# Kernel optimization log

Hardware: AMD Instinct MI355X
Metric: run time of the kernel (lower is better)

The kernel has to match this reference:

```python
import jax, jax.numpy as jnp
import numpy as np

N_NODES = 50000
N_GRAPHS = 64


def gcn_layer(x, W, b, src, dst, norm, n):
    # PyG GCNConv: h = x @ W; aggregate norm-weighted messages at dst; add bias
    h = x @ W
    msg = h[src] * norm[:, None]          # [E_tot, out_dim] gather
    out = jax.ops.segment_sum(msg, dst, num_segments=n)
    return out + b


def to_dense_batch(x, batch, max_num, num_graphs):
    n = x.shape[0]
    counts = jax.ops.segment_sum(jnp.ones((n,), x.dtype), batch, num_segments=num_graphs)
    starts = jnp.concatenate([jnp.zeros((1,), jnp.int32),
                              jnp.cumsum(counts.astype(jnp.int32))[:-1]])
    pos = jnp.arange(n, dtype=jnp.int32) - starts[batch]
    valid = pos < max_num
    b_idx = jnp.where(valid, batch, num_graphs)   # overflow -> dummy row
    p_idx = jnp.where(valid, pos, 0)
    dense = jnp.zeros((num_graphs + 1, max_num, x.shape[1]), x.dtype)
    dense = dense.at[b_idx, p_idx].set(x)
    return dense[:num_graphs]


def setup_inputs() -> dict:
    key = jax.random.key(0)
    ks = jax.random.split(key, 12)
    F0, F2, F3, OUT = 54, 108, 216, 200
    x = jax.random.normal(ks[0], (N_NODES, F0), jnp.float32)
    edge_index = jax.random.randint(ks[1], (2, 800000), 0, N_NODES, jnp.int64)
    batch = jnp.sort(jax.random.randint(ks[2], (N_NODES,), 0, N_GRAPHS, jnp.int64))
    def glorot(k, shp):
        lim = 1.0 / np.sqrt(shp[0])
        return jax.random.uniform(k, shp, jnp.float32, -lim, lim)
    return {
        "x": x, "edge_index": edge_index, "batch": batch, "max_num": 1000,
        "W1": glorot(ks[3], (F0, F0)), "b1": jnp.zeros((F0,), jnp.float32),
        "W2": glorot(ks[4], (F0, F2)), "b2": jnp.zeros((F2,), jnp.float32),
        "W3": glorot(ks[5], (F2, F3)), "b3": jnp.zeros((F3,), jnp.float32),
        "Wf": glorot(ks[6], (F3, OUT)), "bf": glorot(ks[7], (OUT,)),
    }


def reference(x, edge_index, batch, max_num, W1, b1, W2, b2, W3, b3, Wf, bf):
    n = x.shape[0]
    loops = jnp.arange(n, dtype=edge_index.dtype)
    src = jnp.concatenate([edge_index[0], loops])
    dst = jnp.concatenate([edge_index[1], loops])
    # symmetric GCN normalization with self-loops (edge_weight = 1)
    deg = jax.ops.segment_sum(jnp.ones_like(dst, jnp.float32), dst, num_segments=n)
    dinv = jax.lax.rsqrt(deg)  # deg >= 1 due to self-loops
    norm = dinv[src] * dinv[dst]

    h = jax.nn.relu(gcn_layer(x, W1, b1, src, dst, norm, n))
    h = jax.nn.relu(gcn_layer(h, W2, b2, src, dst, norm, n))
    h = jax.nn.relu(gcn_layer(h, W3, b3, src, dst, norm, n))
    h = h @ Wf + bf
    return to_dense_batch(h, batch, max_num, N_GRAPHS)
```

## Files before the change

kernel.cpp:

```cpp
#include <hip/hip_runtime.h>
#include <hip/hip_bf16.h>

#define N_GRAPHS 64

typedef __bf16 bf16x8 __attribute__((ext_vector_type(8)));
typedef float floatx4 __attribute__((ext_vector_type(4)));
typedef unsigned short ushort8v __attribute__((ext_vector_type(8)));

__device__ __forceinline__ float b2f(unsigned short u) {
    union { unsigned int i; float f; } v;
    v.i = ((unsigned int)u) << 16;
    return v.f;
}
__device__ __forceinline__ unsigned short f2b(float f) {
    __hip_bfloat16 h = __float2bfloat16(f);
    return *(unsigned short*)&h;
}


__global__ void k_deg(const int* __restrict__ dst, int* __restrict__ deg, int E) {
    int e = blockIdx.x * blockDim.x + threadIdx.x;
    if (e < E) atomicAdd(&deg[dst[e]], 1);
}

__global__ void k_scan_blocks(const int* __restrict__ deg, int* __restrict__ row_start,
                              int* __restrict__ blk_sums, int N) {
    __shared__ int s[256];
    int t = threadIdx.x;
    int i = blockIdx.x * 256 + t;
    int v = (i < N) ? deg[i] : 0;
    s[t] = v;
    __syncthreads();
    for (int off = 1; off < 256; off <<= 1) {
        int x = (t >= off) ? s[t - off] : 0;
        __syncthreads();
        s[t] += x;
        __syncthreads();
    }
    if (i < N) row_start[i] = s[t] - v;
    if (t == 255) blk_sums[blockIdx.x] = s[255];
}

__global__ void k_scan_tot(const int* __restrict__ blk_sums, int nb, int* __restrict__ blk_off) {
    __shared__ int s[256];
    int t = threadIdx.x;
    int v = (t < nb) ? blk_sums[t] : 0;
    s[t] = v;
    __syncthreads();
    for (int off = 1; off < 256; off <<= 1) {
        int x = (t >= off) ? s[t - off] : 0;
        __syncthreads();
        s[t] += x;
        __syncthreads();
    }
    if (t < nb) blk_off[t] = s[t] - v;
}

__global__ void k_scan_add(int* __restrict__ row_start, const int* __restrict__ blk_off,
                           int* __restrict__ cursor, const int* __restrict__ deg,
                           float* __restrict__ dinv, const int* __restrict__ batch,
                           int* __restrict__ gstarts, int N, int E) {
    int i = blockIdx.x * 256 + threadIdx.x;
    if (i < N) {
        int r = row_start[i] + blk_off[blockIdx.x];
        row_start[i] = r;
        cursor[i] = r;
        dinv[i] = 1.0f / sqrtf((float)(deg[i] + 1));
        int b = batch[i];
        int prev = (i == 0) ? -1 : batch[i - 1];
        for (int g = prev + 1; g <= b; ++g) gstarts[g] = i;
        if (i == N - 1)
            for (int g = b + 1; g <= N_GRAPHS; ++g) gstarts[g] = N;
    }
    if (i == 0) row_start[N] = E;
}

__global__ void k_fill(const int* __restrict__ src, const int* __restrict__ dst,
                       int* __restrict__ cursor, int2* __restrict__ col2,
                       const float* __restrict__ dinv, int E) {
    int e = blockIdx.x * blockDim.x + threadIdx.x;
    if (e < E) {
        int s = src[e];
        int p = atomicAdd(&cursor[dst[e]], 1);
        col2[p] = make_int2(s, __float_as_int(dinv[s]));
    }
}

__device__ __forceinline__ void swz_one(const float* __restrict__ W,
                                        unsigned short* __restrict__ Wsw, int i, int K, int Nn,
                                        int KS) {
    int j = i & 7, lane = (i >> 3) & 63;
    int ks = (i >> 9) % KS, nt = i / (512 * KS);
    int n = nt * 16 + (lane & 15);
    int k = ks * 32 + (lane >> 4) * 8 + j;
    float v = (k < K && n < Nn) ? W[(size_t)k * Nn + n] : 0.f;
    Wsw[i] = f2b(v);
}

#define T_W1 (4 * 2 * 512)
#define T_W2 (8 * 2 * 512)
#define T_W3 (14 * 4 * 512)
#define T_WF (13 * 7 * 512)

__global__ void k_prep(const float* __restrict__ W1, const float* __restrict__ W2,
                       const float* __restrict__ W3, const float* __restrict__ Wf,
                       unsigned short* __restrict__ W1s, unsigned short* __restrict__ W2s,
                       unsigned short* __restrict__ W3s, unsigned short* __restrict__ Wfs,
                       const float* __restrict__ x, unsigned short* __restrict__ xb, int Nn) {
    int i = blockIdx.x * 256 + threadIdx.x;
    if (i < T_W1) swz_one(W1, W1s, i, 54, 54, 2);
    else if (i < T_W1 + T_W2) swz_one(W2, W2s, i - T_W1, 54, 108, 2);
    else if (i < T_W1 + T_W2 + T_W3) swz_one(W3, W3s, i - T_W1 - T_W2, 108, 216, 4);
    else if (i < T_W1 + T_W2 + T_W3 + T_WF)
        swz_one(Wf, Wfs, i - T_W1 - T_W2 - T_W3, 216, 200, 7);
    else {
        int ii = i - (T_W1 + T_W2 + T_W3 + T_WF);
        if (ii < Nn * 64) {
            int n = ii >> 6, c = ii & 63;
            xb[ii] = (c < 54) ? f2b(x[(size_t)n * 54 + c]) : (unsigned short)0;
        }
    }
}


template <int P, int AS, int NODES, int NG>
__device__ __forceinline__ void gatherP(const unsigned short* __restrict__ in,
                                        const int* __restrict__ row_start,
                                        const int2* __restrict__ col2,
                                        const float* __restrict__ dinv,
                                        unsigned short* agg_s, int node0, int N, int t) {
    constexpr int S = P / 8;
    constexpr int G = 32 / S;
    constexpr int RPG = NODES / NG;
    int grp = t >> 5, lane5 = t & 31;
    int j = lane5 / S, cl = lane5 % S;
    int rs_a[RPG], re_a[RPG];
    float dn_a[RPG];
#pragma unroll
    for (int rr = 0; rr < RPG; ++rr) {
        int n = node0 + grp + rr * NG;
        bool valid = n < N;
        rs_a[rr] = valid ? row_start[n] : 0;
        re_a[rr] = valid ? row_start[n + 1] : 0;
        dn_a[rr] = valid ? dinv[n] : 0.f;
    }
#pragma unroll
    for (int rr = 0; rr < RPG; ++rr) {
        int r = grp + rr * NG;
        int n = node0 + r;
        float a[8] = {0.f, 0.f, 0.f, 0.f, 0.f, 0.f, 0.f, 0.f};
        if (n < N) {
            float dn = dn_a[rr];
            if (j == 0) {
                ushort8v u = *((const ushort8v*)(in + (size_t)n * P) + cl);
#pragma unroll
                for (int i = 0; i < 8; ++i) a[i] = dn * b2f(u[i]);
            }
            int re = re_a[rr];
            int e = rs_a[rr] + j;
            for (; e < re; e += 4 * G) {
                int e1 = min(e + G, re - 1);
                int e2 = min(e + 2 * G, re - 1);
                int e3 = min(e + 3 * G, re - 1);
                int2 c0 = col2[e];
                int2 c1 = col2[e1];
                int2 c2 = col2[e2];
                int2 c3 = col2[e3];
                ushort8v v0 = *((const ushort8v*)(in + (size_t)c0.x * P) + cl);
                ushort8v v1 = *((const ushort8v*)(in + (size_t)c1.x * P) + cl);
                ushort8v v2 = *((const ushort8v*)(in + (size_t)c2.x * P) + cl);
                ushort8v v3 = *((const ushort8v*)(in + (size_t)c3.x * P) + cl);
                float d0 = __int_as_float(c0.y);
                float d1 = (e + G < re) ? __int_as_float(c1.y) : 0.f;
                float d2 = (e + 2 * G < re) ? __int_as_float(c2.y) : 0.f;
                float d3 = (e + 3 * G < re) ? __int_as_float(c3.y) : 0.f;
#pragma unroll
                for (int i = 0; i < 8; ++i) {
                    a[i] += d0 * b2f(v0[i]) + d1 * b2f(v1[i]);
                    a[i] += d2 * b2f(v2[i]) + d3 * b2f(v3[i]);
                }
            }
#pragma unroll
            for (int i = 0; i < 8; ++i) a[i] *= dn;
        }
#pragma unroll
        for (int mask = S; mask < 32; mask <<= 1)
#pragma unroll
            for (int i = 0; i < 8; ++i) a[i] += __shfl_xor(a[i], mask, 32);
        if (j == 0) {
            ushort8v rv;
#pragma unroll
            for (int i = 0; i < 8; ++i) rv[i] = f2b(a[i]);
            *((ushort8v*)(agg_s + r * AS) + cl) = rv;
        }
    }
}


template <int P, int FOUT, int FP, int KS, int NT>
__global__ __launch_bounds__(256) void k_layer(
    const unsigned short* __restrict__ in, const int* __restrict__ row_start,
    const int2* __restrict__ col2, const float* __restrict__ dinv,
    const unsigned short* __restrict__ Wsw, const float* __restrict__ bias,
    unsigned short* __restrict__ hout, int N) {
    constexpr int AS = KS * 32 + 8;
    __shared__ __align__(16) unsigned short agg_s[16 * AS];
    int node0 = blockIdx.x * 16;
    int t = threadIdx.x;
    gatherP<P, AS, 16, 8>(in, row_start, col2, dinv, agg_s, node0, N, t);
    __syncthreads();
    int lane = t & 63, wv = t >> 6, m = lane & 15, q = lane >> 4;
    bf16x8 a[KS];
#pragma unroll
    for (int ks = 0; ks < KS; ++ks)
        a[ks] = *(const bf16x8*)(agg_s + m * AS + ks * 32 + q * 8);
    for (int nt = wv; nt < NT; nt += 4) {
        const unsigned short* bp = Wsw + ((size_t)(nt * KS) * 64 + lane) * 8;
        bf16x8 bfr[KS];
#pragma unroll
        for (int ks = 0; ks < KS; ++ks) bfr[ks] = *(const bf16x8*)(bp + ks * 512);
        int fo = nt * 16 + m;
        float bb = (fo < FOUT) ? bias[fo] : 0.f;
        floatx4 c = {0.f, 0.f, 0.f, 0.f};
#pragma unroll
        for (int ks = 0; ks < KS; ++ks)
            c = __builtin_amdgcn_mfma_f32_16x16x32_bf16(a[ks], bfr[ks], c, 0, 0, 0);
#pragma unroll
        for (int r = 0; r < 4; ++r) {
            int n = node0 + q * 4 + r;
            if (n < N) hout[(size_t)n * FP + fo] = f2b(fmaxf(c[r] + bb, 0.f));
        }
    }
}


__global__ __launch_bounds__(256) void k_l3f(
    const unsigned short* __restrict__ h2, const int* __restrict__ row_start,
    const int2* __restrict__ col2, const float* __restrict__ dinv,
    const unsigned short* __restrict__ W3s, const float* __restrict__ b3,
    const unsigned short* __restrict__ Wfs, const float* __restrict__ bfv,
    const int* __restrict__ batch, const int* __restrict__ gstarts, float* __restrict__ out,
    int N, int mn) {
    constexpr int AS = 136, HS = 232;
    __shared__ __align__(16) unsigned short smem[32 * HS];
    unsigned short* agg_s = smem;
    unsigned short* h3_s = smem;
    int node0 = blockIdx.x * 32;
    int t = threadIdx.x;
    gatherP<128, AS, 32, 8>(h2, row_start, col2, dinv, agg_s, node0, N, t);
    __syncthreads();
    int lane = t & 63, wv = t >> 6, m = lane & 15, q = lane >> 4;
    bf16x8 a1[2][4];
#pragma unroll
    for (int mt = 0; mt < 2; ++mt)
#pragma unroll
        for (int ks = 0; ks < 4; ++ks)
            a1[mt][ks] = *(const bf16x8*)(agg_s + (mt * 16 + m) * AS + ks * 32 + q * 8);
    __syncthreads();
    for (int nt = wv; nt < 14; nt += 4) {
        const unsigned short* bp = W3s + ((size_t)(nt * 4) * 64 + lane) * 8;
        bf16x8 bf0 = *(const bf16x8*)(bp);
        bf16x8 bf1 = *(const bf16x8*)(bp + 512);
        bf16x8 bf2 = *(const bf16x8*)(bp + 1024);
        bf16x8 bf3 = *(const bf16x8*)(bp + 1536);
        int fo = nt * 16 + m;
        float bb = (fo < 216) ? b3[fo] : 0.f;
#pragma unroll
        for (int mt = 0; mt < 2; ++mt) {
            floatx4 c = {0.f, 0.f, 0.f, 0.f};
            c = __builtin_amdgcn_mfma_f32_16x16x32_bf16(a1[mt][0], bf0, c, 0, 0, 0);
            c = __builtin_amdgcn_mfma_f32_16x16x32_bf16(a1[mt][1], bf1, c, 0, 0, 0);
            c = __builtin_amdgcn_mfma_f32_16x16x32_bf16(a1[mt][2], bf2, c, 0, 0, 0);
            c = __builtin_amdgcn_mfma_f32_16x16x32_bf16(a1[mt][3], bf3, c, 0, 0, 0);
#pragma unroll
            for (int r = 0; r < 4; ++r) {
                int row = mt * 16 + q * 4 + r;
                h3_s[row * HS + fo] = f2b(fmaxf(c[r] + bb, 0.f));
            }
        }
    }
    __syncthreads();
    bf16x8 a2[2][7];
#pragma unroll
    for (int mt = 0; mt < 2; ++mt)
#pragma unroll
        for (int ks = 0; ks < 7; ++ks)
            a2[mt][ks] = *(const bf16x8*)(h3_s + (mt * 16 + m) * HS + ks * 32 + q * 8);
    for (int nt = wv; nt < 13; nt += 4) {
        const unsigned short* bp = Wfs + ((size_t)(nt * 7) * 64 + lane) * 8;
        bf16x8 bfr[7];
#pragma unroll
        for (int ks = 0; ks < 7; ++ks) bfr[ks] = *(const bf16x8*)(bp + ks * 512);
        int fo = nt * 16 + m;
        if (fo >= 200) continue;
        float bb = bfv[fo];
#pragma unroll
        for (int mt = 0; mt < 2; ++mt) {
            floatx4 c = {0.f, 0.f, 0.f, 0.f};
#pragma unroll
            for (int ks = 0; ks < 7; ++ks)
                c = __builtin_amdgcn_mfma_f32_16x16x32_bf16(a2[mt][ks], bfr[ks], c, 0, 0, 0);
#pragma unroll
            for (int r = 0; r < 4; ++r) {
                int n = node0 + mt * 16 + q * 4 + r;
                if (n < N) {
                    int b = batch[n];
                    int pos = n - gstarts[b];
                    if (pos >= 0 && pos < mn)
                        out[((size_t)b * mn + pos) * 200 + fo] = c[r] + bb;
                }
            }
        }
    }
}

extern "C" void kernel_launch(void* const* d_in, const int* in_sizes, int n_in,
                              void* d_out, int out_size, void* d_ws, size_t ws_size,
                              hipStream_t stream) {
    const float* x = (const float*)d_in[0];
    const int* ei = (const int*)d_in[1];
    const int* batch = (const int*)d_in[2];
    const float* W1 = (const float*)d_in[4];
    const float* b1 = (const float*)d_in[5];
    const float* W2 = (const float*)d_in[6];
    const float* b2 = (const float*)d_in[7];
    const float* W3 = (const float*)d_in[8];
    const float* b3 = (const float*)d_in[9];
    const float* Wf = (const float*)d_in[10];
    const float* bfv = (const float*)d_in[11];
    float* out = (float*)d_out;

    const int N = in_sizes[2];
    const int E = in_sizes[1] / 2;
    const int mn = out_size / (N_GRAPHS * 200);
    const int* src = ei;
    const int* dst = ei + E;

    char* w = (char*)d_ws;
    auto alloc = [&](size_t bytes) {
        void* p = (void*)w;
        w += (bytes + 255) & ~(size_t)255;
        return p;
    };
    int* deg = (int*)alloc((size_t)N * 4);
    int* row_start = (int*)alloc((size_t)(N + 1) * 4);
    int* blk_sums = (int*)alloc(256 * 4);
    int* blk_off = (int*)alloc(256 * 4);
    int* cursor = (int*)alloc((size_t)N * 4);
    int2* col2 = (int2*)alloc((size_t)E * 8);
    float* dinv = (float*)alloc((size_t)N * 4);
    int* gstarts = (int*)alloc((N_GRAPHS + 1) * 4);
    unsigned short* xb = (unsigned short*)alloc((size_t)N * 64 * 2);
    unsigned short* h1 = (unsigned short*)alloc((size_t)N * 64 * 2);
    unsigned short* h2 = (unsigned short*)alloc((size_t)N * 128 * 2);
    unsigned short* W1s = (unsigned short*)alloc((size_t)T_W1 * 2);
    unsigned short* W2s = (unsigned short*)alloc((size_t)T_W2 * 2);
    unsigned short* W3s = (unsigned short*)alloc((size_t)T_W3 * 2);
    unsigned short* Wfs = (unsigned short*)alloc((size_t)T_WF * 2);
    (void)ws_size;

    hipMemsetAsync(deg, 0, (size_t)N * 4, stream);
    hipMemsetAsync(d_out, 0, (size_t)out_size * sizeof(float), stream);

    int NB = (N + 255) / 256;
    k_deg<<<(E + 255) / 256, 256, 0, stream>>>(dst, deg, E);
    k_scan_blocks<<<NB, 256, 0, stream>>>(deg, row_start, blk_sums, N);
    k_scan_tot<<<1, 256, 0, stream>>>(blk_sums, NB, blk_off);
    k_scan_add<<<NB, 256, 0, stream>>>(row_start, blk_off, cursor, deg, dinv, batch, gstarts,
                                       N, E);
    k_fill<<<(E + 255) / 256, 256, 0, stream>>>(src, dst, cursor, col2, dinv, E);
    int prep_total = T_W1 + T_W2 + T_W3 + T_WF + N * 64;
    k_prep<<<(prep_total + 255) / 256, 256, 0, stream>>>(W1, W2, W3, Wf, W1s, W2s, W3s, Wfs,
                                                         x, xb, N);

    int NBL16 = (N + 15) / 16;
    k_layer<64, 54, 64, 2, 4><<<NBL16, 256, 0, stream>>>(xb, row_start, col2, dinv, W1s, b1,
                                                         h1, N);
    k_layer<64, 108, 128, 2, 8><<<NBL16, 256, 0, stream>>>(h1, row_start, col2, dinv, W2s,
                                                           b2, h2, N);
    int NBL32 = (N + 31) / 32;
    k_l3f<<<NBL32, 256, 0, stream>>>(h2, row_start, col2, dinv, W3s, b3, Wfs, bfv, batch,
                                     gstarts, out, N, mn);
}
```

Baseline: 304.5 us.

## Merge degree count with weight prep and fill with padding-only output zeroing

Fuses the edge degree-count kernel with the weight swizzle/x conversion kernel into one launch, and fuses the CSR fill kernel with a new zeroing pass that clears only the padded tail rows of each graph in the dense output. This replaces a full-output memset with zeroing of just the rows the final layer does not write, and drops two launches. It relies on the final kernel writing every valid row, since those rows are no longer pre-zeroed.

```diff
diff --git a/kernel.cpp b/kernel.cpp
--- a/kernel.cpp
+++ b/kernel.cpp
@@ -17,11 +17,6 @@
     return *(unsigned short*)&h;
 }
 
-
-__global__ void k_deg(const int* __restrict__ dst, int* __restrict__ deg, int E) {
-    int e = blockIdx.x * blockDim.x + threadIdx.x;
-    if (e < E) atomicAdd(&deg[dst[e]], 1);
-}
 
 __global__ void k_scan_blocks(const int* __restrict__ deg, int* __restrict__ row_start,
                               int* __restrict__ blk_sums, int N) {
@@ -75,17 +70,6 @@
     if (i == 0) row_start[N] = E;
 }
 
-__global__ void k_fill(const int* __restrict__ src, const int* __restrict__ dst,
-                       int* __restrict__ cursor, int2* __restrict__ col2,
-                       const float* __restrict__ dinv, int E) {
-    int e = blockIdx.x * blockDim.x + threadIdx.x;
-    if (e < E) {
-        int s = src[e];
-        int p = atomicAdd(&cursor[dst[e]], 1);
-        col2[p] = make_int2(s, __float_as_int(dinv[s]));
-    }
-}
-
 __device__ __forceinline__ void swz_one(const float* __restrict__ W,
                                         unsigned short* __restrict__ Wsw, int i, int K, int Nn,
                                         int KS) {
@@ -102,12 +86,19 @@
 #define T_W3 (14 * 4 * 512)
 #define T_WF (13 * 7 * 512)
 
-__global__ void k_prep(const float* __restrict__ W1, const float* __restrict__ W2,
-                       const float* __restrict__ W3, const float* __restrict__ Wf,
-                       unsigned short* __restrict__ W1s, unsigned short* __restrict__ W2s,
-                       unsigned short* __restrict__ W3s, unsigned short* __restrict__ Wfs,
-                       const float* __restrict__ x, unsigned short* __restrict__ xb, int Nn) {
-    int i = blockIdx.x * 256 + threadIdx.x;
+__global__ void k_deg_prep(const int* __restrict__ dst, int* __restrict__ deg, int E, int EB,
+                           const float* __restrict__ W1, const float* __restrict__ W2,
+                           const float* __restrict__ W3, const float* __restrict__ Wf,
+                           unsigned short* __restrict__ W1s, unsigned short* __restrict__ W2s,
+                           unsigned short* __restrict__ W3s, unsigned short* __restrict__ Wfs,
+                           const float* __restrict__ x, unsigned short* __restrict__ xb,
+                           int Nn) {
+    if ((int)blockIdx.x < EB) {
+        int e = blockIdx.x * 256 + threadIdx.x;
+        if (e < E) atomicAdd(&deg[dst[e]], 1);
+        return;
+    }
+    int i = (blockIdx.x - EB) * 256 + threadIdx.x;
     if (i < T_W1) swz_one(W1, W1s, i, 54, 54, 2);
     else if (i < T_W1 + T_W2) swz_one(W2, W2s, i - T_W1, 54, 108, 2);
     else if (i < T_W1 + T_W2 + T_W3) swz_one(W3, W3s, i - T_W1 - T_W2, 108, 216, 4);
@@ -120,6 +111,30 @@
             xb[ii] = (c < 54) ? f2b(x[(size_t)n * 54 + c]) : (unsigned short)0;
         }
     }
+}
+
+__global__ void k_fill_zero(const int* __restrict__ src, const int* __restrict__ dst,
+                            int* __restrict__ cursor, int2* __restrict__ col2,
+                            const float* __restrict__ dinv, int E, int EB,
+                            const int* __restrict__ gstarts, float* __restrict__ out,
+                            int mn) {
+    if ((int)blockIdx.x < EB) {
+        int e = blockIdx.x * 256 + threadIdx.x;
+        if (e < E) {
+            int s = src[e];
+            int p = atomicAdd(&cursor[dst[e]], 1);
+            col2[p] = make_int2(s, __float_as_int(dinv[s]));
+        }
+        return;
+    }
+    int z = blockIdx.x - EB;
+    int g = z >> 3, c8 = z & 7;
+    int cnt = gstarts[g + 1] - gstarts[g];
+    if (cnt > mn) cnt = mn;
+    float4* base = (float4*)(out + ((size_t)g * mn + cnt) * 200);
+    int total4 = (mn - cnt) * 50;
+    for (int i = c8 * 256 + threadIdx.x; i < total4; i += 8 * 256)
+        base[i] = make_float4(0.f, 0.f, 0.f, 0.f);
 }
 
 
@@ -360,18 +375,20 @@
     (void)ws_size;
 
     hipMemsetAsync(deg, 0, (size_t)N * 4, stream);
-    hipMemsetAsync(d_out, 0, (size_t)out_size * sizeof(float), stream);
+
+    int EB = (E + 255) / 256;
+    int prep_total = T_W1 + T_W2 + T_W3 + T_WF + N * 64;
+    int PB = (prep_total + 255) / 256;
+    k_deg_prep<<<EB + PB, 256, 0, stream>>>(dst, deg, E, EB, W1, W2, W3, Wf, W1s, W2s, W3s,
+                                            Wfs, x, xb, N);
 
     int NB = (N + 255) / 256;
-    k_deg<<<(E + 255) / 256, 256, 0, stream>>>(dst, deg, E);
     k_scan_blocks<<<NB, 256, 0, stream>>>(deg, row_start, blk_sums, N);
     k_scan_tot<<<1, 256, 0, stream>>>(blk_sums, NB, blk_off);
     k_scan_add<<<NB, 256, 0, stream>>>(row_start, blk_off, cursor, deg, dinv, batch, gstarts,
                                        N, E);
-    k_fill<<<(E + 255) / 256, 256, 0, stream>>>(src, dst, cursor, col2, dinv, E);
-    int prep_total = T_W1 + T_W2 + T_W3 + T_WF + N * 64;
-    k_prep<<<(prep_total + 255) / 256, 256, 0, stream>>>(W1, W2, W3, Wf, W1s, W2s, W3s, Wfs,
-                                                         x, xb, N);
+    k_fill_zero<<<EB + 8 * N_GRAPHS, 256, 0, stream>>>(src, dst, cursor, col2, dinv, E, EB,
+                                                       gstarts, out, mn);
 
     int NBL16 = (N + 15) / 16;
     k_layer<64, 54, 64, 2, 4><<<NBL16, 256, 0, stream>>>(xb, row_start, col2, dinv, W1s, b1,
```

Result: faster. 296.3 us (-2.7%).
